# Optimization experiments

Measured on AMD Instinct MI355X. Metric: run time of the kernel, lower is better.

## Reference

```python
import jax, jax.numpy as jnp
import numpy as np

DEPTH = 2
DIM = 512
HEADS = 8
DH = 64
INNER = HEADS * DH
MLP = 2048
B = 2
N = 2048
EPS = 1e-6
NEG = -float(np.finfo(np.float32).max)
SCALE = DH ** -0.5


def setup_inputs() -> dict:
    key = jax.random.key(0)
    ks = jax.random.split(key, 8)
    inp = {
        'x': jax.random.normal(ks[0], (B, N, DIM), dtype=jnp.float32),
        'mask': jax.random.randint(ks[1], (B, N), 0, 2, dtype=jnp.int32),
        'qkv_w': 0.02 * jax.random.normal(ks[2], (DEPTH, DIM, 3 * INNER), dtype=jnp.float32),
        'out_w': 0.02 * jax.random.normal(ks[3], (DEPTH, INNER, DIM), dtype=jnp.float32),
        'out_b': jnp.zeros((DEPTH, DIM), dtype=jnp.float32),
        'ff_w1': 0.02 * jax.random.normal(ks[4], (DEPTH, DIM, MLP), dtype=jnp.float32),
        'ff_b1': jnp.zeros((DEPTH, MLP), dtype=jnp.float32),
        'ff_w2': 0.02 * jax.random.normal(ks[5], (DEPTH, MLP, DIM), dtype=jnp.float32),
        'ff_b2': jnp.zeros((DEPTH, DIM), dtype=jnp.float32),
        'ad1_w': jnp.ones((DEPTH, B * DIM), dtype=jnp.float32),
        'ad1_b': jnp.zeros((DEPTH, B * DIM), dtype=jnp.float32),
        'ad2_w': jnp.ones((DEPTH, B * DIM), dtype=jnp.float32),
        'ad2_b': jnp.zeros((DEPTH, B * DIM), dtype=jnp.float32),
    }
    return inp


def adain(x, w, b):
    # AdaptiveInstanceNorm2d: batch_norm over channels (B*D), spatial dim N, training=True
    # -> per-(b, d) mean/biased-var over N, affine params of shape (B*D,) -> (B,1,D)
    mu = jnp.mean(x, axis=1, keepdims=True)
    var = jnp.var(x, axis=1, keepdims=True)  # biased variance, as in batch_norm
    xn = (x - mu) * jax.lax.rsqrt(var + EPS)
    b_sz, _, d = x.shape
    return xn * w.reshape(b_sz, 1, d) + b.reshape(b_sz, 1, d)


def attention(x, mask2d, qkv_w, out_w, out_b):
    b_sz, n, _ = x.shape
    qkv = x @ qkv_w  # [B,N,3*INNER]
    q, k, v = jnp.split(qkv, 3, axis=-1)

    def split_heads(t):
        return t.reshape(b_sz, n, HEADS, DH).transpose(0, 2, 1, 3)  # [B,H,N,D]

    q, k, v = split_heads(q), split_heads(k), split_heads(v)
    dots = jnp.einsum('bhnd,bhmd->bhnm', q, k) * SCALE  # [B,H,N,N]
    dots = jnp.where(mask2d[:, None] == 0, NEG, dots)
    attn = jax.nn.softmax(dots, axis=-1)
    out = jnp.einsum('bhnm,bhmd->bhnd', attn, v)
    out = out.transpose(0, 2, 1, 3).reshape(b_sz, n, INNER)
    return out @ out_w + out_b


def feedforward(x, w1, b1, w2, b2):
    h = jax.nn.gelu(x @ w1 + b1, approximate=False)  # torch nn.GELU default = exact erf
    return h @ w2 + b2


def reference(x, mask, qkv_w, out_w, out_b, ff_w1, ff_b1, ff_w2, ff_b2,
              ad1_w, ad1_b, ad2_w, ad2_b):
    mask2d = mask[:, :, None] * mask[:, None, :]  # [B,N,N]
    for l in range(DEPTH):
        h = adain(x, ad1_w[l], ad1_b[l])
        x = attention(h, mask2d, qkv_w[l], out_w[l], out_b[l]) + x
        h = adain(x, ad2_w[l], ad2_b[l])
        x = feedforward(h, ff_w1[l], ff_b1[l], ff_w2[l], ff_b2[l]) + x
    return x
```

## Files before the change

### kernel.cpp

```cpp
#include <hip/hip_runtime.h>
#include <hip/hip_bf16.h>

#define DEPTHL 2
#define DIMM   512
#define NHEADS 8
#define DHH    64
#define INNERD 512
#define MLPD   2048
#define BB     2
#define SEQL   2048
#define ROWS   (BB*SEQL)
#define MNEG   (-1.0e38f)
#define SCLQ   0.18033688f
#define NSPLIT 4
#define KPS    (SEQL / NSPLIT)
#define NCH    128

typedef __attribute__((ext_vector_type(4))) float f32x4;
typedef __attribute__((ext_vector_type(8))) __bf16 bf16x8;

#define GLDS16(g, l) __builtin_amdgcn_global_load_lds((const __attribute__((address_space(1))) void*)(g), (__attribute__((address_space(3))) void*)(l), 16, 0, 0)

__device__ __forceinline__ unsigned short f2bf(float f) {
  union { float f; unsigned int u; } v; v.f = f;
  unsigned int r = v.u + 0x7fffu + ((v.u >> 16) & 1u);
  return (unsigned short)(r >> 16);
}
__device__ __forceinline__ float bf2f(unsigned short h) {
  union { unsigned int u; float f; } v; v.u = ((unsigned int)h) << 16; return v.f;
}
__device__ __forceinline__ unsigned int cvtpk(float a, float b) {
  unsigned int r;
  asm("v_cvt_pk_bf16_f32 %0, %1, %2" : "=v"(r) : "v"(a), "v"(b));
  return r;
}

__global__ __launch_bounds__(256) void wtrans(const float* __restrict__ wsrc,
                                              unsigned short* __restrict__ wdst,
                                              int K, int N) {
  __shared__ float t[32][33];
  const float* src = wsrc + (size_t)blockIdx.z * K * N;
  unsigned short* dst = wdst + (size_t)blockIdx.z * K * N;
  int k0 = blockIdx.x * 32, n0 = blockIdx.y * 32;
  int tx = threadIdx.x & 31, ty = threadIdx.x >> 5;
#pragma unroll
  for (int j = 0; j < 32; j += 8)
    t[ty + j][tx] = src[(size_t)(k0 + ty + j) * N + n0 + tx];
  __syncthreads();
#pragma unroll
  for (int j = 0; j < 32; j += 8)
    dst[(size_t)(n0 + ty + j) * K + k0 + tx] = f2bf(t[tx][ty + j]);
}

__global__ __launch_bounds__(512) void adain_p1(const float* __restrict__ x,
                                                float* __restrict__ p1, float* __restrict__ p2) {
  int d = threadIdx.x, c = blockIdx.x, b = blockIdx.y;
  const float* xp = x + ((size_t)b * SEQL + c * 16) * DIMM + d;
  float s = 0.f, s2 = 0.f;
#pragma unroll
  for (int i = 0; i < 16; ++i) { float v = xp[(size_t)i * DIMM]; s += v; s2 += v * v; }
  p1[(b * NCH + c) * DIMM + d] = s;
  p2[(b * NCH + c) * DIMM + d] = s2;
}

__global__ __launch_bounds__(512) void adain_p2(const float* __restrict__ p1, const float* __restrict__ p2,
                                                const float* __restrict__ w, const float* __restrict__ bi,
                                                float* __restrict__ alpha, float* __restrict__ beta) {
  __shared__ float redA[8][64], redB[8][64];
  int b = blockIdx.x, dg = blockIdx.y;
  int dl = threadIdx.x & 63, seg = threadIdx.x >> 6;
  int d = dg * 64 + dl;
  float s = 0.f, s2 = 0.f;
#pragma unroll
  for (int i = 0; i < 16; ++i) {
    int c = seg * 16 + i;
    s += p1[(b * NCH + c) * DIMM + d];
    s2 += p2[(b * NCH + c) * DIMM + d];
  }
  redA[seg][dl] = s; redB[seg][dl] = s2;
  __syncthreads();
  if (seg == 0) {
#pragma unroll
    for (int i = 1; i < 8; ++i) { s += redA[i][dl]; s2 += redB[i][dl]; }
    float mean = s * (1.0f / SEQL);
    float var = s2 * (1.0f / SEQL) - mean * mean;
    float a = w[b * DIMM + d] * rsqrtf(var + 1e-6f);
    alpha[b * DIMM + d] = a;
    beta[b * DIMM + d] = bi[b * DIMM + d] - mean * a;
  }
}

__global__ __launch_bounds__(256) void adain_apply(const float* __restrict__ x,
                                                   const float* __restrict__ alpha, const float* __restrict__ beta,
                                                   unsigned short* __restrict__ hb) {
  int idx = (blockIdx.x * 256 + threadIdx.x) * 4;
  int d = idx & (DIMM - 1);
  int b = idx >> 20;
  f32x4 xv = *(const f32x4*)&x[idx];
  f32x4 av = *(const f32x4*)&alpha[b * DIMM + d];
  f32x4 bv = *(const f32x4*)&beta[b * DIMM + d];
  *(uint2*)&hb[idx] = make_uint2(cvtpk(xv[0] * av[0] + bv[0], xv[1] * av[1] + bv[1]),
                                 cvtpk(xv[2] * av[2] + bv[2], xv[3] * av[3] + bv[3]));
}

__global__ __launch_bounds__(256) void maskbuild(const int* __restrict__ mask, float* __restrict__ maskadd) {
  int i = blockIdx.x * 256 + threadIdx.x;
  maskadd[i] = mask[i] ? 0.f : MNEG;
}

template <int EPI, int BN>
__global__ __launch_bounds__(256)
void gemm_k(const unsigned short* __restrict__ A,
            const unsigned short* __restrict__ Wt,
            const float* __restrict__ bias,
            const float* __restrict__ resid,
            float* __restrict__ outF,
            unsigned short* __restrict__ outB,
            unsigned short* __restrict__ part,
            unsigned short* __restrict__ qg4,
            unsigned short* __restrict__ kg4,
            unsigned short* __restrict__ vt4,
            int N, int Kt) {
  constexpr int NI = BN / 32;
  __shared__ __align__(16) unsigned short As[2][128 * 32];
  __shared__ __align__(16) unsigned short Bs[2][BN * 32];
  const int tid = threadIdx.x;
  const int w = tid >> 6, lane = tid & 63;

  unsigned int f = blockIdx.y * gridDim.x + blockIdx.x;
  unsigned int grp = f & 7u, idx = f >> 3;
  unsigned int rpx = gridDim.y >> 3;
  unsigned int by = grp * rpx + idx / gridDim.x;
  unsigned int bx = idx % gridDim.x;

  const int bm = by * 128, bn = bx * BN;
  const int wm = (w >> 1) * 64, wn = (w & 1) * (BN / 2);

  const int nsplit = gridDim.z, sp = blockIdx.z;
  const int Kc = Kt / nsplit;
  const int kbeg = sp * Kc, kend = kbeg + Kc;

  f32x4 acc[4][NI] = {};

  auto stage = [&](int buf, int k0) {
#pragma unroll
    for (int j = 0; j < 2; ++j) {
      int r = w * 32 + (lane >> 2) + j * 16;
      int cl = (lane & 3) ^ ((r >> 1) & 3);
      GLDS16(A + (size_t)(bm + r) * Kt + k0 + cl * 8, &As[buf][(w * 32 + j * 16) * 32]);
    }
    if (BN == 128) {
#pragma unroll
      for (int j = 0; j < 2; ++j) {
        int r = w * 32 + (lane >> 2) + j * 16;
        int cl = (lane & 3) ^ ((r >> 1) & 3);
        GLDS16(Wt + (size_t)(bn + r) * Kt + k0 + cl * 8, &Bs[buf][(w * 32 + j * 16) * 32]);
      }
    } else {
      int r = w * 16 + (lane >> 2);
      int cl = (lane & 3) ^ ((r >> 1) & 3);
      GLDS16(Wt + (size_t)(bn + r) * Kt + k0 + cl * 8, &Bs[buf][(w * 16) * 32]);
    }
  };

  stage(0, kbeg);
  __syncthreads();
  int cur = 0;

  for (int k0 = kbeg; k0 < kend; k0 += 32) {
    if (k0 + 32 < kend) stage(cur ^ 1, k0 + 32);
    bf16x8 af[4], bfr[NI];
#pragma unroll
    for (int i = 0; i < 4; ++i) {
      int ar = wm + i * 16 + (lane & 15);
      int ac = (lane >> 4) ^ ((ar >> 1) & 3);
      af[i] = *(const bf16x8*)&As[cur][ar * 32 + ac * 8];
    }
#pragma unroll
    for (int i = 0; i < NI; ++i) {
      int br = wn + i * 16 + (lane & 15);
      int bc = (lane >> 4) ^ ((br >> 1) & 3);
      bfr[i] = *(const bf16x8*)&Bs[cur][br * 32 + bc * 8];
    }
#pragma unroll
    for (int mi = 0; mi < 4; ++mi)
#pragma unroll
      for (int ni = 0; ni < NI; ++ni)
        acc[mi][ni] = __builtin_amdgcn_mfma_f32_16x16x32_bf16(af[mi], bfr[ni], acc[mi][ni], 0, 0, 0);
    __syncthreads();
    cur ^= 1;
  }

  const size_t MN = (size_t)gridDim.y * 128 * N;
#pragma unroll
  for (int mi = 0; mi < 4; ++mi) {
#pragma unroll
    for (int ni = 0; ni < NI; ++ni) {
#pragma unroll
      for (int r = 0; r < 4; ++r) {
        int row = bm + wm + mi * 16 + (lane >> 4) * 4 + r;
        int col = bn + wn + ni * 16 + (lane & 15);
        float v = acc[mi][ni][r];
        if (EPI == 4) {
          int brow = row >> 11, n = row & (SEQL - 1);
          int sec = col >> 9, h = (col >> 6) & 7, dh = col & 63;
          int bh = brow * 8 + h;
          if (sec == 0) qg4[((size_t)bh * SEQL + n) * DHH + dh] = f2bf(v * SCLQ);
          else if (sec == 1) kg4[((size_t)bh * SEQL + n) * DHH + dh] = f2bf(v);
          else vt4[((size_t)bh * DHH + dh) * SEQL + n] = f2bf(v);
        } else {
          size_t o = (size_t)row * N + col;
          if (EPI == 3) {
            part[(size_t)sp * MN + o] = f2bf(v);
          } else {
            if (bias) v += bias[col];
            if (EPI == 1) v = 0.5f * v * (1.0f + erff(v * 0.70710678118f));
            if (EPI == 2) outF[o] = v + resid[o];
            else outB[o] = f2bf(v);
          }
        }
      }
    }
  }
}

template <int NS>
__global__ __launch_bounds__(256) void comb_k(const unsigned short* __restrict__ part,
                                              const float* __restrict__ bias,
                                              const float* __restrict__ resid,
                                              float* __restrict__ outF) {
  size_t idx = ((size_t)blockIdx.x * 256 + threadIdx.x) * 4;
  int col = (int)(idx & 511);
  float a0 = 0.f, a1 = 0.f, a2 = 0.f, a3 = 0.f;
#pragma unroll
  for (int s = 0; s < NS; ++s) {
    uint2 v = *(const uint2*)&part[(size_t)s * ROWS * 512 + idx];
    a0 += bf2f(v.x & 0xffff); a1 += bf2f(v.x >> 16);
    a2 += bf2f(v.y & 0xffff); a3 += bf2f(v.y >> 16);
  }
  f32x4 b = *(const f32x4*)&bias[col];
  f32x4 rs = *(const f32x4*)&resid[idx];
  f32x4 o;
  o[0] = a0 + b[0] + rs[0]; o[1] = a1 + b[1] + rs[1];
  o[2] = a2 + b[2] + rs[2]; o[3] = a3 + b[3] + rs[3];
  *(f32x4*)&outF[idx] = o;
}

__global__ __launch_bounds__(256) void vmean_k(const unsigned short* __restrict__ vt,
                                               float* __restrict__ vmean) {
  __shared__ float red[256];
  int bh = blockIdx.x, t = threadIdx.x;
  int d = blockIdx.y * 8 + (t >> 5), seg = t & 31;
  const unsigned short* p = vt + ((size_t)bh * 64 + d) * SEQL + seg * 64;
  float s = 0.f;
#pragma unroll
  for (int i = 0; i < 16; ++i) {
    uint2 v = *(const uint2*)&p[i * 4];
    s += bf2f(v.x & 0xffff) + bf2f(v.x >> 16) + bf2f(v.y & 0xffff) + bf2f(v.y >> 16);
  }
  red[t] = s;
  __syncthreads();
  if (t < 8) {
    float a = 0.f;
#pragma unroll
    for (int i = 0; i < 32; ++i) a += red[t * 32 + i];
    vmean[bh * 64 + blockIdx.y * 8 + t] = a * (1.0f / SEQL);
  }
}

__global__ __launch_bounds__(256, 4)
void attn_split(const unsigned short* __restrict__ qg,
                const unsigned short* __restrict__ kg,
                const unsigned short* __restrict__ vtg,
                const float* __restrict__ maskadd,
                unsigned short* __restrict__ opart,
                float* __restrict__ lpart) {
  __shared__ __align__(16) unsigned short Ks[64 * 64];
  __shared__ __align__(16) unsigned short Vts[64 * 64];
  __shared__ __align__(16) unsigned short Ps[4 * 32 * 64];
  const int tid = threadIdx.x, w = tid >> 6, lane = tid & 63;
  const int g = lane >> 4, c = lane & 15;
  const int bh = blockIdx.y, b = bh >> 3;
  const int qt = blockIdx.x;
  const int split = blockIdx.z;
  const int kv0 = split * KPS;
  const int q0 = qt * 128 + w * 32;
  const float* maskb = maskadd + b * SEQL;

  bf16x8 qf0[2], qf1[2];
#pragma unroll
  for (int kb = 0; kb < 2; ++kb) {
    qf0[kb] = *(const bf16x8*)&qg[((size_t)bh * SEQL + q0 + c) * DHH + kb * 32 + g * 8];
    qf1[kb] = *(const bf16x8*)&qg[((size_t)bh * SEQL + q0 + 16 + c) * DHH + kb * 32 + g * 8];
  }

  const __bf16 one1 = (__bf16)1.0f;
  const bf16x8 ones = {one1, one1, one1, one1, one1, one1, one1, one1};

  f32x4 o0[4] = {}, o1[4] = {};
  f32x4 lones0 = {}, lones1 = {};
  unsigned short* myP = &Ps[w * 2048];

  for (int kt = 0; kt < KPS / 64; ++kt) {
#pragma unroll
    for (int j = 0; j < 2; ++j) {
      int r = w * 16 + j * 8 + (lane >> 3);
      int cl = (lane & 7) ^ (r & 7);
      GLDS16(kg + ((size_t)bh * SEQL + kv0 + kt * 64 + r) * DHH + cl * 8, &Ks[(w * 16 + j * 8) * 64]);
      GLDS16(vtg + ((size_t)bh * DHH + r) * SEQL + kv0 + kt * 64 + cl * 8, &Vts[(w * 16 + j * 8) * 64]);
    }
    __syncthreads();

    f32x4 sT0[4], sT1[4];
#pragma unroll
    for (int nt = 0; nt < 4; ++nt) {
      f32x4 mk = *(const f32x4*)&maskb[kv0 + kt * 64 + nt * 16 + g * 4];
      sT0[nt] = mk;
      sT1[nt] = mk;
    }
#pragma unroll
    for (int nt = 0; nt < 4; ++nt) {
#pragma unroll
      for (int kb = 0; kb < 2; ++kb) {
        int kr = nt * 16 + c;
        int cs = (kb * 4 + g) ^ (kr & 7);
        bf16x8 kf = *(const bf16x8*)&Ks[kr * 64 + cs * 8];
        sT0[nt] = __builtin_amdgcn_mfma_f32_16x16x32_bf16(kf, qf0[kb], sT0[nt], 0, 0, 0);
        sT1[nt] = __builtin_amdgcn_mfma_f32_16x16x32_bf16(kf, qf1[kb], sT1[nt], 0, 0, 0);
      }
    }

#pragma unroll
    for (int nt = 0; nt < 4; ++nt) {
      int swz = (((nt * 2 + (g >> 1)) ^ (c & 7)) << 3) + ((g & 1) << 2);
      {
        float pv0 = exp2f(sT0[nt][0]), pv1 = exp2f(sT0[nt][1]);
        float pv2 = exp2f(sT0[nt][2]), pv3 = exp2f(sT0[nt][3]);
        *(uint2*)(myP + c * 64 + swz) = make_uint2(cvtpk(pv0, pv1), cvtpk(pv2, pv3));
      }
      {
        float pv0 = exp2f(sT1[nt][0]), pv1 = exp2f(sT1[nt][1]);
        float pv2 = exp2f(sT1[nt][2]), pv3 = exp2f(sT1[nt][3]);
        *(uint2*)(myP + (16 + c) * 64 + swz) = make_uint2(cvtpk(pv0, pv1), cvtpk(pv2, pv3));
      }
    }

#pragma unroll
    for (int kb = 0; kb < 2; ++kb) {
      int ps = ((kb * 4 + g) ^ (c & 7)) << 3;
      bf16x8 pf0 = *(const bf16x8*)&myP[c * 64 + ps];
      bf16x8 pf1 = *(const bf16x8*)&myP[(16 + c) * 64 + ps];
      lones0 = __builtin_amdgcn_mfma_f32_16x16x32_bf16(pf0, ones, lones0, 0, 0, 0);
      lones1 = __builtin_amdgcn_mfma_f32_16x16x32_bf16(pf1, ones, lones1, 0, 0, 0);
#pragma unroll
      for (int ni = 0; ni < 4; ++ni) {
        int vr = ni * 16 + c;
        int vc = (kb * 4 + g) ^ (vr & 7);
        bf16x8 vf = *(const bf16x8*)&Vts[vr * 64 + vc * 8];
        o0[ni] = __builtin_amdgcn_mfma_f32_16x16x32_bf16(pf0, vf, o0[ni], 0, 0, 0);
        o1[ni] = __builtin_amdgcn_mfma_f32_16x16x32_bf16(pf1, vf, o1[ni], 0, 0, 0);
      }
    }
    __syncthreads();
  }

  const size_t pb = ((size_t)split * 16 + bh) * SEQL;
#pragma unroll
  for (int ni = 0; ni < 4; ++ni) {
#pragma unroll
    for (int r = 0; r < 4; ++r) {
      opart[(pb + q0 + g * 4 + r) * DHH + ni * 16 + c] = f2bf(o0[ni][r]);
      opart[(pb + q0 + 16 + g * 4 + r) * DHH + ni * 16 + c] = f2bf(o1[ni][r]);
    }
  }
  if (c == 0) {
#pragma unroll
    for (int r = 0; r < 4; ++r) {
      lpart[pb + q0 + g * 4 + r] = lones0[r];
      lpart[pb + q0 + 16 + g * 4 + r] = lones1[r];
    }
  }
}

__global__ __launch_bounds__(256) void attn_combine(const unsigned short* __restrict__ opart,
                                                    const float* __restrict__ lpart,
                                                    const float* __restrict__ maskadd,
                                                    const float* __restrict__ vmean,
                                                    unsigned short* __restrict__ ctx) {
  int idx = blockIdx.x * 256 + threadIdx.x;
  int dq = idx & 7;
  int q = (idx >> 3) & (SEQL - 1);
  int bh = idx >> 14;
  int d0 = dq * 8;
  int b = bh >> 3, h = bh & 7;
  float ov[8] = {};
  float L = 0.f;
#pragma unroll
  for (int s = 0; s < NSPLIT; ++s) {
    size_t base = ((size_t)s * 16 + bh) * SEQL + q;
    L += lpart[base];
    uint4 v = *(const uint4*)&opart[base * DHH + d0];
    ov[0] += bf2f(v.x & 0xffff); ov[1] += bf2f(v.x >> 16);
    ov[2] += bf2f(v.y & 0xffff); ov[3] += bf2f(v.y >> 16);
    ov[4] += bf2f(v.z & 0xffff); ov[5] += bf2f(v.z >> 16);
    ov[6] += bf2f(v.w & 0xffff); ov[7] += bf2f(v.w >> 16);
  }
  float r = 1.0f / L;
  if (maskadd[b * SEQL + q] != 0.f) {
#pragma unroll
    for (int i = 0; i < 8; ++i) ov[i] = vmean[bh * 64 + d0 + i];
  } else {
#pragma unroll
    for (int i = 0; i < 8; ++i) ov[i] *= r;
  }
  *(uint4*)&ctx[((size_t)(b * SEQL + q)) * INNERD + h * 64 + d0] =
      make_uint4(cvtpk(ov[0], ov[1]), cvtpk(ov[2], ov[3]), cvtpk(ov[4], ov[5]), cvtpk(ov[6], ov[7]));
}

extern "C" void kernel_launch(void* const* d_in, const int* in_sizes, int n_in,
                              void* d_out, int out_size, void* d_ws, size_t ws_size,
                              hipStream_t stream) {
  (void)in_sizes; (void)n_in; (void)out_size;
  const float* x_in = (const float*)d_in[0];
  const int* mask = (const int*)d_in[1];
  const float* qkv_w = (const float*)d_in[2];
  const float* out_w = (const float*)d_in[3];
  const float* out_b = (const float*)d_in[4];
  const float* ff_w1 = (const float*)d_in[5];
  const float* ff_b1 = (const float*)d_in[6];
  const float* ff_w2 = (const float*)d_in[7];
  const float* ff_b2 = (const float*)d_in[8];
  const float* ad1w = (const float*)d_in[9];
  const float* ad1b = (const float*)d_in[10];
  const float* ad2w = (const float*)d_in[11];
  const float* ad2b = (const float*)d_in[12];

  char* ws = (char*)d_ws;
  size_t off = 0;
  auto alloc = [&](size_t bytes) {
    char* p = ws + off;
    off = (off + bytes + 255) & ~(size_t)255;
    return p;
  };
  unsigned short* wtQ = (unsigned short*)alloc((size_t)DEPTHL * 1536 * 512 * 2);
  unsigned short* wtO = (unsigned short*)alloc((size_t)DEPTHL * 512 * 512 * 2);
  unsigned short* wtF1 = (unsigned short*)alloc((size_t)DEPTHL * 2048 * 512 * 2);
  unsigned short* wtF2 = (unsigned short*)alloc((size_t)DEPTHL * 512 * 2048 * 2);
  float* xc = (float*)alloc((size_t)ROWS * DIMM * 4);
  unsigned short* hbf = (unsigned short*)alloc((size_t)ROWS * DIMM * 2);
  char* region2 = alloc((size_t)4 * 16 * SEQL * DHH * 2);
  unsigned short* qb = (unsigned short*)region2;
  unsigned short* kb = qb + (size_t)16 * SEQL * DHH;
  unsigned short* vtb = kb + (size_t)16 * SEQL * DHH;
  unsigned short* ctxb = vtb + (size_t)16 * SEQL * DHH;
  unsigned short* h1bf = (unsigned short*)region2;
  float* p1 = (float*)alloc((size_t)BB * NCH * DIMM * 4);
  float* p2 = (float*)alloc((size_t)BB * NCH * DIMM * 4);
  float* alpha = (float*)alloc((size_t)BB * DIMM * 4);
  float* beta = (float*)alloc((size_t)BB * DIMM * 4);
  float* maskadd = (float*)alloc((size_t)BB * SEQL * 4);
  unsigned short* opart = (unsigned short*)alloc((size_t)NSPLIT * 16 * SEQL * DHH * 2);
  float* lpart = (float*)alloc((size_t)NSPLIT * 16 * SEQL * 4);
  float* vmean = (float*)alloc((size_t)16 * 64 * 4);
  unsigned short* part = (unsigned short*)alloc((size_t)4 * ROWS * 512 * 2);
  const bool fits = off <= ws_size;

  wtrans<<<dim3(512 / 32, 1536 / 32, DEPTHL), 256, 0, stream>>>(qkv_w, wtQ, 512, 1536);
  wtrans<<<dim3(512 / 32, 512 / 32, DEPTHL), 256, 0, stream>>>(out_w, wtO, 512, 512);
  wtrans<<<dim3(512 / 32, 2048 / 32, DEPTHL), 256, 0, stream>>>(ff_w1, wtF1, 512, 2048);
  wtrans<<<dim3(2048 / 32, 512 / 32, DEPTHL), 256, 0, stream>>>(ff_w2, wtF2, 2048, 512);
  maskbuild<<<BB * SEQL / 256, 256, 0, stream>>>(mask, maskadd);

  for (int l = 0; l < DEPTHL; ++l) {
    const float* xr = (l == 0) ? x_in : xc;
    adain_p1<<<dim3(NCH, BB), 512, 0, stream>>>(xr, p1, p2);
    adain_p2<<<dim3(BB, 8), 512, 0, stream>>>(p1, p2, ad1w + l * BB * DIMM, ad1b + l * BB * DIMM, alpha, beta);
    adain_apply<<<2048, 256, 0, stream>>>(xr, alpha, beta, hbf);
    gemm_k<4, 64><<<dim3(1536 / 64, ROWS / 128), 256, 0, stream>>>(
        hbf, wtQ + (size_t)l * 1536 * 512, nullptr, nullptr, nullptr, nullptr, nullptr,
        qb, kb, vtb, 1536, 512);
    vmean_k<<<dim3(16, 8), 256, 0, stream>>>(vtb, vmean);
    attn_split<<<dim3(SEQL / 128, 16, NSPLIT), 256, 0, stream>>>(qb, kb, vtb, maskadd, opart, lpart);
    attn_combine<<<16 * SEQL * 8 / 256, 256, 0, stream>>>(opart, lpart, maskadd, vmean, ctxb);
    if (fits) {
      gemm_k<3, 64><<<dim3(512 / 64, ROWS / 128, 2), 256, 0, stream>>>(
          ctxb, wtO + (size_t)l * 512 * 512, nullptr, nullptr, nullptr, nullptr, part,
          nullptr, nullptr, nullptr, 512, 512);
      comb_k<2><<<ROWS * 512 / 1024, 256, 0, stream>>>(part, out_b + l * DIMM, xr, xc);
    } else {
      gemm_k<2, 64><<<dim3(512 / 64, ROWS / 128), 256, 0, stream>>>(
          ctxb, wtO + (size_t)l * 512 * 512, out_b + l * DIMM, xr, xc, nullptr, nullptr,
          nullptr, nullptr, nullptr, 512, 512);
    }
    adain_p1<<<dim3(NCH, BB), 512, 0, stream>>>(xc, p1, p2);
    adain_p2<<<dim3(BB, 8), 512, 0, stream>>>(p1, p2, ad2w + l * BB * DIMM, ad2b + l * BB * DIMM, alpha, beta);
    adain_apply<<<2048, 256, 0, stream>>>(xc, alpha, beta, hbf);
    gemm_k<1, 64><<<dim3(2048 / 64, ROWS / 128), 256, 0, stream>>>(
        hbf, wtF1 + (size_t)l * 2048 * 512, ff_b1 + l * MLPD, nullptr, nullptr, h1bf, nullptr,
        nullptr, nullptr, nullptr, 2048, 512);
    float* xout = (l == DEPTHL - 1) ? (float*)d_out : xc;
    if (fits) {
      gemm_k<3, 64><<<dim3(512 / 64, ROWS / 128, 4), 256, 0, stream>>>(
          h1bf, wtF2 + (size_t)l * 512 * 2048, nullptr, nullptr, nullptr, nullptr, part,
          nullptr, nullptr, nullptr, 512, 2048);
      comb_k<4><<<ROWS * 512 / 1024, 256, 0, stream>>>(part, ff_b2 + l * DIMM, xc, xout);
    } else {
      gemm_k<2, 64><<<dim3(512 / 64, ROWS / 128), 256, 0, stream>>>(
          h1bf, wtF2 + (size_t)l * 512 * 2048, ff_b2 + l * DIMM, xc, xout, nullptr, nullptr,
          nullptr, nullptr, nullptr, 512, 2048);
    }
  }
}
```

Measured before the change: 286.1 us.

## Use 32x32x16 MFMA in split attention and keep P in registers via permlane32 swap

Rewrites the split-KV attention kernel to use 32x32x16 bf16 MFMA tiles instead of 16x16x32, so each wave computes a 32-query by 32-key score tile per instruction. The exponentiated probabilities are packed to bf16 and rearranged across lane halves with v_permlane32_swap so they can feed the PV MFMA directly. This removes the per-wave LDS staging buffer for P and its store/load round trip. It also changes the accumulator layout and the output store pattern. In exchange it needs larger 16-wide accumulators and depends on the register layout mapping being exactly right.

```diff
diff --git a/kernel.cpp b/kernel.cpp
--- a/kernel.cpp
+++ b/kernel.cpp
@@ -17,6 +17,7 @@
 #define NCH    128
 
 typedef __attribute__((ext_vector_type(4))) float f32x4;
+typedef __attribute__((ext_vector_type(16))) float f32x16;
 typedef __attribute__((ext_vector_type(8))) __bf16 bf16x8;
 
 #define GLDS16(g, l) __builtin_amdgcn_global_load_lds((const __attribute__((address_space(1))) void*)(g), (__attribute__((address_space(3))) void*)(l), 16, 0, 0)
@@ -277,9 +278,8 @@
                 float* __restrict__ lpart) {
   __shared__ __align__(16) unsigned short Ks[64 * 64];
   __shared__ __align__(16) unsigned short Vts[64 * 64];
-  __shared__ __align__(16) unsigned short Ps[4 * 32 * 64];
   const int tid = threadIdx.x, w = tid >> 6, lane = tid & 63;
-  const int g = lane >> 4, c = lane & 15;
+  const int h = lane >> 5, ln = lane & 31;
   const int bh = blockIdx.y, b = bh >> 3;
   const int qt = blockIdx.x;
   const int split = blockIdx.z;
@@ -287,19 +287,15 @@
   const int q0 = qt * 128 + w * 32;
   const float* maskb = maskadd + b * SEQL;
 
-  bf16x8 qf0[2], qf1[2];
-#pragma unroll
-  for (int kb = 0; kb < 2; ++kb) {
-    qf0[kb] = *(const bf16x8*)&qg[((size_t)bh * SEQL + q0 + c) * DHH + kb * 32 + g * 8];
-    qf1[kb] = *(const bf16x8*)&qg[((size_t)bh * SEQL + q0 + 16 + c) * DHH + kb * 32 + g * 8];
-  }
+  bf16x8 qf[4];
+#pragma unroll
+  for (int dhc = 0; dhc < 4; ++dhc)
+    qf[dhc] = *(const bf16x8*)&qg[((size_t)bh * SEQL + q0 + ln) * DHH + dhc * 16 + h * 8];
 
   const __bf16 one1 = (__bf16)1.0f;
   const bf16x8 ones = {one1, one1, one1, one1, one1, one1, one1, one1};
 
-  f32x4 o0[4] = {}, o1[4] = {};
-  f32x4 lones0 = {}, lones1 = {};
-  unsigned short* myP = &Ps[w * 2048];
+  f32x16 o0 = {}, o1 = {}, lones = {};
 
   for (int kt = 0; kt < KPS / 64; ++kt) {
 #pragma unroll
@@ -311,74 +307,62 @@
     }
     __syncthreads();
 
-    f32x4 sT0[4], sT1[4];
-#pragma unroll
-    for (int nt = 0; nt < 4; ++nt) {
-      f32x4 mk = *(const f32x4*)&maskb[kv0 + kt * 64 + nt * 16 + g * 4];
-      sT0[nt] = mk;
-      sT1[nt] = mk;
-    }
-#pragma unroll
-    for (int nt = 0; nt < 4; ++nt) {
+#pragma unroll
+    for (int st = 0; st < 2; ++st) {
+      const int kr = st * 32 + ln;
+      f32x16 sT;
+#pragma unroll
+      for (int uq = 0; uq < 4; ++uq) {
+        f32x4 mk = *(const f32x4*)&maskb[kv0 + kt * 64 + st * 32 + uq * 8 + h * 4];
+        sT[uq * 4 + 0] = mk[0]; sT[uq * 4 + 1] = mk[1];
+        sT[uq * 4 + 2] = mk[2]; sT[uq * 4 + 3] = mk[3];
+      }
+#pragma unroll
+      for (int dhc = 0; dhc < 4; ++dhc) {
+        bf16x8 kf = *(const bf16x8*)&Ks[kr * 64 + (((dhc << 1) + h) ^ (kr & 7)) * 8];
+        sT = __builtin_amdgcn_mfma_f32_32x32x16_bf16(kf, qf[dhc], sT, 0, 0, 0);
+      }
+      float p[16];
+#pragma unroll
+      for (int u = 0; u < 16; ++u) p[u] = exp2f(sT[u]);
 #pragma unroll
       for (int kb = 0; kb < 2; ++kb) {
-        int kr = nt * 16 + c;
-        int cs = (kb * 4 + g) ^ (kr & 7);
-        bf16x8 kf = *(const bf16x8*)&Ks[kr * 64 + cs * 8];
-        sT0[nt] = __builtin_amdgcn_mfma_f32_16x16x32_bf16(kf, qf0[kb], sT0[nt], 0, 0, 0);
-        sT1[nt] = __builtin_amdgcn_mfma_f32_16x16x32_bf16(kf, qf1[kb], sT1[nt], 0, 0, 0);
+        unsigned int wa0 = cvtpk(p[kb * 8 + 0], p[kb * 8 + 1]);
+        unsigned int wa1 = cvtpk(p[kb * 8 + 2], p[kb * 8 + 3]);
+        unsigned int wb0 = cvtpk(p[kb * 8 + 4], p[kb * 8 + 5]);
+        unsigned int wb1 = cvtpk(p[kb * 8 + 6], p[kb * 8 + 7]);
+        asm volatile("v_permlane32_swap_b32 %0, %1" : "+v"(wa0), "+v"(wb0));
+        asm volatile("v_permlane32_swap_b32 %0, %1" : "+v"(wa1), "+v"(wb1));
+        union { unsigned int w4[4]; bf16x8 v; } pfu;
+        pfu.w4[0] = wa0; pfu.w4[1] = wa1; pfu.w4[2] = wb0; pfu.w4[3] = wb1;
+        bf16x8 pf = pfu.v;
+        lones = __builtin_amdgcn_mfma_f32_32x32x16_bf16(pf, ones, lones, 0, 0, 0);
+        {
+          int vr = ln;
+          bf16x8 vf = *(const bf16x8*)&Vts[vr * 64 + (((st * 4 + kb * 2 + h) ^ (vr & 7)) << 3)];
+          o0 = __builtin_amdgcn_mfma_f32_32x32x16_bf16(pf, vf, o0, 0, 0, 0);
+        }
+        {
+          int vr = 32 + ln;
+          bf16x8 vf = *(const bf16x8*)&Vts[vr * 64 + (((st * 4 + kb * 2 + h) ^ (vr & 7)) << 3)];
+          o1 = __builtin_amdgcn_mfma_f32_32x32x16_bf16(pf, vf, o1, 0, 0, 0);
+        }
       }
     }
-
-#pragma unroll
-    for (int nt = 0; nt < 4; ++nt) {
-      int swz = (((nt * 2 + (g >> 1)) ^ (c & 7)) << 3) + ((g & 1) << 2);
-      {
-        float pv0 = exp2f(sT0[nt][0]), pv1 = exp2f(sT0[nt][1]);
-        float pv2 = exp2f(sT0[nt][2]), pv3 = exp2f(sT0[nt][3]);
-        *(uint2*)(myP + c * 64 + swz) = make_uint2(cvtpk(pv0, pv1), cvtpk(pv2, pv3));
-      }
-      {
-        float pv0 = exp2f(sT1[nt][0]), pv1 = exp2f(sT1[nt][1]);
-        float pv2 = exp2f(sT1[nt][2]), pv3 = exp2f(sT1[nt][3]);
-        *(uint2*)(myP + (16 + c) * 64 + swz) = make_uint2(cvtpk(pv0, pv1), cvtpk(pv2, pv3));
-      }
-    }
-
-#pragma unroll
-    for (int kb = 0; kb < 2; ++kb) {
-      int ps = ((kb * 4 + g) ^ (c & 7)) << 3;
-      bf16x8 pf0 = *(const bf16x8*)&myP[c * 64 + ps];
-      bf16x8 pf1 = *(const bf16x8*)&myP[(16 + c) * 64 + ps];
-      lones0 = __builtin_amdgcn_mfma_f32_16x16x32_bf16(pf0, ones, lones0, 0, 0, 0);
-      lones1 = __builtin_amdgcn_mfma_f32_16x16x32_bf16(pf1, ones, lones1, 0, 0, 0);
-#pragma unroll
-      for (int ni = 0; ni < 4; ++ni) {
-        int vr = ni * 16 + c;
-        int vc = (kb * 4 + g) ^ (vr & 7);
-        bf16x8 vf = *(const bf16x8*)&Vts[vr * 64 + vc * 8];
-        o0[ni] = __builtin_amdgcn_mfma_f32_16x16x32_bf16(pf0, vf, o0[ni], 0, 0, 0);
-        o1[ni] = __builtin_amdgcn_mfma_f32_16x16x32_bf16(pf1, vf, o1[ni], 0, 0, 0);
-      }
-    }
     __syncthreads();
   }
 
   const size_t pb = ((size_t)split * 16 + bh) * SEQL;
 #pragma unroll
-  for (int ni = 0; ni < 4; ++ni) {
-#pragma unroll
-    for (int r = 0; r < 4; ++r) {
-      opart[(pb + q0 + g * 4 + r) * DHH + ni * 16 + c] = f2bf(o0[ni][r]);
-      opart[(pb + q0 + 16 + g * 4 + r) * DHH + ni * 16 + c] = f2bf(o1[ni][r]);
-    }
-  }
-  if (c == 0) {
-#pragma unroll
-    for (int r = 0; r < 4; ++r) {
-      lpart[pb + q0 + g * 4 + r] = lones0[r];
-      lpart[pb + q0 + 16 + g * 4 + r] = lones1[r];
-    }
+  for (int u = 0; u < 16; ++u) {
+    int q = q0 + (u & 3) + 8 * (u >> 2) + 4 * h;
+    opart[(pb + q) * DHH + ln] = f2bf(o0[u]);
+    opart[(pb + q) * DHH + 32 + ln] = f2bf(o1[u]);
+  }
+  if (ln == 0) {
+#pragma unroll
+    for (int u = 0; u < 16; ++u)
+      lpart[pb + q0 + (u & 3) + 8 * (u >> 2) + 4 * h] = lones[u];
   }
 }
 
```

New measurement: 288.6 us. Within noise of the previous version (+0.9%).
